# Performance work log

Measured on AMD Instinct MI355X. Metric: run time of the kernel, lower is better.

## Reference

```python
import jax, jax.numpy as jnp
import numpy as np
from jax import lax

B = 4_194_304  # batch rows
H = 7          # hidden width
N_MID = 19     # fc2..fc20


def setup_inputs() -> dict:
    key = jax.random.key(0)
    ks = jax.random.split(key, 7)
    x = jax.random.normal(ks[0], (B, 2), dtype=jnp.float32)
    # torch Linear default init scale ~ 1/sqrt(fan_in); use small uniform-like normals
    W1 = jax.random.normal(ks[1], (H, 2), dtype=jnp.float32) / jnp.sqrt(2.0)
    b1 = jax.random.normal(ks[2], (H,), dtype=jnp.float32) * 0.1
    Wm = jax.random.normal(ks[3], (N_MID, H, H), dtype=jnp.float32) / jnp.sqrt(float(H))
    bm = jax.random.normal(ks[4], (N_MID, H), dtype=jnp.float32) * 0.1
    Wo = jax.random.normal(ks[5], (2, H), dtype=jnp.float32) / jnp.sqrt(float(H))
    bo = jax.random.normal(ks[6], (2,), dtype=jnp.float32) * 0.1
    return {"x": x, "W1": W1, "b1": b1, "Wm": Wm, "bm": bm, "Wo": Wo, "bo": bo}


def reference(x, W1, b1, Wm, bm, Wo, bo):
    # fc1 + ELU
    h = jax.nn.elu(x @ W1.T + b1)  # [B, 7]

    # fc2..fc20 (19 identical-shape Linear(7,7)+ELU layers) via scan
    def step(h, wb):
        w, b = wb  # w: [7,7], b: [7]
        return jax.nn.elu(h @ w.T + b), None

    h, _ = lax.scan(step, h, (Wm, bm))

    # fc21 + log_softmax
    logits = h @ Wo.T + bo  # [B, 2]
    return jax.nn.log_softmax(logits, axis=1)
```

## Files before the change

kernel.cpp:

```cpp
#include <hip/hip_runtime.h>
#include <hip/hip_bf16.h>

#define HH 7
#define NMID 19

__global__ __launch_bounds__(256) void net_mlp_kernel(
    const float* __restrict__ x,
    const float* __restrict__ W1, const float* __restrict__ b1,
    const float* __restrict__ Wm, const float* __restrict__ bm,
    const float* __restrict__ Wo, const float* __restrict__ bo,
    float* __restrict__ out, int B)
{
    int i = blockIdx.x * blockDim.x + threadIdx.x;
    if (i >= B) return;

    const float2 xin = reinterpret_cast<const float2*>(x)[i];

    float h[HH];

#pragma unroll
    for (int j = 0; j < HH; ++j) {
        float a = fmaf(xin.x, W1[j * 2 + 0], fmaf(xin.y, W1[j * 2 + 1], b1[j]));
        h[j] = (a > 0.0f) ? a : (__expf(a) - 1.0f);
    }

#pragma unroll
    for (int l = 0; l < NMID; ++l) {
        const float* __restrict__ W = Wm + l * (HH * HH);
        const float* __restrict__ b = bm + l * HH;
        float nh[HH];
#pragma unroll
        for (int j = 0; j < HH; ++j) {
            float a = b[j];
#pragma unroll
            for (int k = 0; k < HH; ++k)
                a = fmaf(h[k], W[j * HH + k], a);
            nh[j] = (a > 0.0f) ? a : (__expf(a) - 1.0f);
        }
#pragma unroll
        for (int j = 0; j < HH; ++j) h[j] = nh[j];
    }

    float l0 = bo[0], l1 = bo[1];
#pragma unroll
    for (int k = 0; k < HH; ++k) {
        l0 = fmaf(h[k], Wo[k], l0);
        l1 = fmaf(h[k], Wo[HH + k], l1);
    }
    float m = fmaxf(l0, l1);
    float z = m + __logf(__expf(l0 - m) + __expf(l1 - m));

    float2 o;
    o.x = l0 - z;
    o.y = l1 - z;
    reinterpret_cast<float2*>(out)[i] = o;
}

extern "C" void kernel_launch(void* const* d_in, const int* in_sizes, int n_in,
                              void* d_out, int out_size, void* d_ws, size_t ws_size,
                              hipStream_t stream) {
    const float* x  = (const float*)d_in[0];
    const float* W1 = (const float*)d_in[1];
    const float* b1 = (const float*)d_in[2];
    const float* Wm = (const float*)d_in[3];
    const float* bm = (const float*)d_in[4];
    const float* Wo = (const float*)d_in[5];
    const float* bo = (const float*)d_in[6];
    float* out = (float*)d_out;

    const int B = in_sizes[0] / 2;
    const int block = 256;
    const int grid = (B + block - 1) / block;
    net_mlp_kernel<<<grid, block, 0, stream>>>(x, W1, b1, Wm, bm, Wo, bo, out, B);
}
```

Baseline: 237.8 us.

## Use packed fp16 dot2 for MLP layers with prepacked weights and 4 rows/thread

Adds a prep kernel that converts the weights to packed half2 padded to 8 columns in the workspace. The main kernel keeps activations as packed fp16 and computes each layer with v_dot2 fp16-to-fp32 instructions, which cuts FMA count roughly in half. Each thread now processes 4 rows strided across the batch for ILP. The risks are fp16 precision loss across 20 layers, an extra kernel launch, and no tail handling when B is not divisible by 1024.

```diff
diff --git a/kernel.cpp b/kernel.cpp
--- a/kernel.cpp
+++ b/kernel.cpp
@@ -1,59 +1,133 @@
 #include <hip/hip_runtime.h>
 #include <hip/hip_bf16.h>
+#include <stdint.h>
 
 #define HH 7
 #define NMID 19
+#define RPT 4
+#define BLOCK 256
 
-__global__ __launch_bounds__(256) void net_mlp_kernel(
+typedef _Float16 half2_t __attribute__((ext_vector_type(2)));
+
+__device__ __forceinline__ uint32_t pack_h2(float a, float b) {
+    return __builtin_bit_cast(uint32_t, __builtin_amdgcn_cvt_pkrtz(a, b));
+}
+
+
+__global__ void prep_kernel(const float* __restrict__ W1, const float* __restrict__ b1,
+                            const float* __restrict__ Wm, const float* __restrict__ bm,
+                            const float* __restrict__ Wo, const float* __restrict__ bo,
+                            uint32_t* __restrict__ ws)
+{
+    const int t = threadIdx.x;
+    float* wsf = (float*)ws;
+
+    if (t < 8) {
+        float w0 = (t < HH) ? W1[t * 2 + 0] : 0.f;
+        float w1 = (t < HH) ? W1[t * 2 + 1] : 0.f;
+        ws[t] = pack_h2(w0, w1);
+        wsf[8 + t] = (t < HH) ? b1[t] : 0.f;
+
+        int r = t >> 2, p = t & 3;
+        int k0 = 2 * p, k1 = 2 * p + 1;
+        float o0 = (k0 < HH) ? Wo[r * HH + k0] : 0.f;
+        float o1 = (k1 < HH) ? Wo[r * HH + k1] : 0.f;
+        ws[776 + t] = pack_h2(o0, o1);
+    }
+    if (t < 2) wsf[784 + t] = bo[t];
+
+    for (int e = t; e < NMID * 8 * 4; e += BLOCK) {
+        int l = e >> 5;
+        int j = (e >> 2) & 7;
+        int p = e & 3;
+        float w0 = 0.f, w1 = 0.f;
+        if (j < HH) {
+            int k0 = 2 * p, k1 = 2 * p + 1;
+            if (k0 < HH) w0 = Wm[(l * HH + j) * HH + k0];
+            if (k1 < HH) w1 = Wm[(l * HH + j) * HH + k1];
+        }
+        ws[16 + e] = pack_h2(w0, w1);
+    }
+    for (int e = t; e < NMID * 8; e += BLOCK) {
+        int l = e >> 3, j = e & 7;
+        wsf[624 + e] = (j < HH) ? bm[l * HH + j] : 0.f;
+    }
+}
+
+__device__ __forceinline__ float elu_f32(float a) {
+    return (a > 0.f) ? a : (__expf(a) - 1.f);
+}
+
+__device__ __forceinline__ half2_t as_h2(uint32_t u) {
+    return __builtin_bit_cast(half2_t, u);
+}
+
+__global__ __launch_bounds__(BLOCK) void net_main(
     const float* __restrict__ x,
-    const float* __restrict__ W1, const float* __restrict__ b1,
-    const float* __restrict__ Wm, const float* __restrict__ bm,
-    const float* __restrict__ Wo, const float* __restrict__ bo,
-    float* __restrict__ out, int B)
+    const uint32_t* __restrict__ ws,
+    float* __restrict__ out, int nthreads)
 {
-    int i = blockIdx.x * blockDim.x + threadIdx.x;
-    if (i >= B) return;
+    const int t = blockIdx.x * blockDim.x + threadIdx.x;
+    const int stride = nthreads;
+    const float* __restrict__ wsf = (const float*)ws;
 
-    const float2 xin = reinterpret_cast<const float2*>(x)[i];
+    float2 xin[RPT];
+#pragma unroll
+    for (int u = 0; u < RPT; ++u)
+        xin[u] = reinterpret_cast<const float2*>(x)[t + u * stride];
 
-    float h[HH];
+    uint32_t h[RPT][4];
 
 #pragma unroll
-    for (int j = 0; j < HH; ++j) {
-        float a = fmaf(xin.x, W1[j * 2 + 0], fmaf(xin.y, W1[j * 2 + 1], b1[j]));
-        h[j] = (a > 0.0f) ? a : (__expf(a) - 1.0f);
+    for (int u = 0; u < RPT; ++u) {
+        uint32_t xv = pack_h2(xin[u].x, xin[u].y);
+        float e[HH];
+#pragma unroll
+        for (int j = 0; j < HH; ++j) {
+            float a = __builtin_amdgcn_fdot2(as_h2(xv), as_h2(ws[j]), wsf[8 + j], false);
+            e[j] = elu_f32(a);
+        }
+        h[u][0] = pack_h2(e[0], e[1]);
+        h[u][1] = pack_h2(e[2], e[3]);
+        h[u][2] = pack_h2(e[4], e[5]);
+        h[u][3] = pack_h2(e[6], 0.f);
     }
 
 #pragma unroll
     for (int l = 0; l < NMID; ++l) {
-        const float* __restrict__ W = Wm + l * (HH * HH);
-        const float* __restrict__ b = bm + l * HH;
-        float nh[HH];
+        const uint32_t* __restrict__ wl = ws + 16 + l * 32;
+        const float* __restrict__ bl = wsf + 624 + l * 8;
 #pragma unroll
-        for (int j = 0; j < HH; ++j) {
-            float a = b[j];
+        for (int u = 0; u < RPT; ++u) {
+            float e[HH];
 #pragma unroll
-            for (int k = 0; k < HH; ++k)
-                a = fmaf(h[k], W[j * HH + k], a);
-            nh[j] = (a > 0.0f) ? a : (__expf(a) - 1.0f);
+            for (int j = 0; j < HH; ++j) {
+                float acc = bl[j];
+#pragma unroll
+                for (int p = 0; p < 4; ++p)
+                    acc = __builtin_amdgcn_fdot2(as_h2(h[u][p]), as_h2(wl[j * 4 + p]), acc, false);
+                e[j] = elu_f32(acc);
+            }
+            h[u][0] = pack_h2(e[0], e[1]);
+            h[u][1] = pack_h2(e[2], e[3]);
+            h[u][2] = pack_h2(e[4], e[5]);
+            h[u][3] = pack_h2(e[6], 0.f);
         }
-#pragma unroll
-        for (int j = 0; j < HH; ++j) h[j] = nh[j];
     }
 
-    float l0 = bo[0], l1 = bo[1];
 #pragma unroll
-    for (int k = 0; k < HH; ++k) {
-        l0 = fmaf(h[k], Wo[k], l0);
-        l1 = fmaf(h[k], Wo[HH + k], l1);
+    for (int u = 0; u < RPT; ++u) {
+        float l0 = wsf[784], l1 = wsf[785];
+#pragma unroll
+        for (int p = 0; p < 4; ++p) {
+            l0 = __builtin_amdgcn_fdot2(as_h2(h[u][p]), as_h2(ws[776 + p]), l0, false);
+            l1 = __builtin_amdgcn_fdot2(as_h2(h[u][p]), as_h2(ws[776 + 4 + p]), l1, false);
+        }
+        float m = fmaxf(l0, l1);
+        float z = m + __logf(__expf(l0 - m) + __expf(l1 - m));
+        float2 o; o.x = l0 - z; o.y = l1 - z;
+        reinterpret_cast<float2*>(out)[t + u * stride] = o;
     }
-    float m = fmaxf(l0, l1);
-    float z = m + __logf(__expf(l0 - m) + __expf(l1 - m));
-
-    float2 o;
-    o.x = l0 - z;
-    o.y = l1 - z;
-    reinterpret_cast<float2*>(out)[i] = o;
 }
 
 extern "C" void kernel_launch(void* const* d_in, const int* in_sizes, int n_in,
@@ -67,9 +141,12 @@
     const float* Wo = (const float*)d_in[5];
     const float* bo = (const float*)d_in[6];
     float* out = (float*)d_out;
+    uint32_t* ws = (uint32_t*)d_ws;
 
     const int B = in_sizes[0] / 2;
-    const int block = 256;
-    const int grid = (B + block - 1) / block;
-    net_mlp_kernel<<<grid, block, 0, stream>>>(x, W1, b1, Wm, bm, Wo, bo, out, B);
+    const int nthreads = B / RPT;
+    const int grid = nthreads / BLOCK;
+
+    prep_kernel<<<1, BLOCK, 0, stream>>>(W1, b1, Wm, bm, Wo, bo, ws);
+    net_main<<<grid, BLOCK, 0, stream>>>(x, ws, out, nthreads);
 }
```

Result: slower. 265.8 us (+11.8%).
